# Optimization experiments

Measured on AMD Instinct MI355X. Metric: run time of the kernel, lower is better.

The kernel has to match this reference:

```python
import jax, jax.numpy as jnp
import numpy as np


def _gru_layer(x, h0, W_ih, W_hh, b_ih, b_hh):
    """PyTorch-convention GRU layer.
    x: [B, T, F], h0: [B, H], W_ih: [3H, F], W_hh: [3H, H], biases: [3H].
    Gate order (torch): r, z, n.  Returns (out [B,T,H], hT [B,H]).
    """
    # Precompute input projections for all timesteps in one big GEMM.
    gx = jnp.einsum('btf,gf->btg', x, W_ih) + b_ih  # [B, T, 3H]
    gx = jnp.swapaxes(gx, 0, 1)  # [T, B, 3H] for scan

    def step(h, gx_t):
        gh = h @ W_hh.T + b_hh                      # [B, 3H]
        xr, xz, xn = jnp.split(gx_t, 3, axis=-1)
        hr, hz, hn = jnp.split(gh, 3, axis=-1)
        r = jax.nn.sigmoid(xr + hr)
        z = jax.nn.sigmoid(xz + hz)
        n = jnp.tanh(xn + r * hn)
        h_new = (1.0 - z) * n + z * h
        return h_new, h_new

    hT, outs = jax.lax.scan(step, h0, gx)
    return jnp.swapaxes(outs, 0, 1), hT  # [B, T, H], [B, H]


def setup_inputs() -> dict:
    key = jax.random.key(0)
    ks = jax.random.split(key, 12)
    B, T, F, H, O = 256, 2000, 80, 64, 29
    s = 1.0 / np.sqrt(H)  # torch GRU/Linear init scale ~ U(-1/sqrt(H), 1/sqrt(H))
    u = lambda k, shp: jax.random.uniform(k, shp, jnp.float32, -s, s)
    return {
        'x': jax.random.normal(ks[0], (B, T, F), jnp.float32),
        'h': jnp.zeros((2, B, H), jnp.float32),
        'W_ih0': u(ks[1], (3 * H, F)),
        'W_hh0': u(ks[2], (3 * H, H)),
        'b_ih0': u(ks[3], (3 * H,)),
        'b_hh0': u(ks[4], (3 * H,)),
        'W_ih1': u(ks[5], (3 * H, H)),
        'W_hh1': u(ks[6], (3 * H, H)),
        'b_ih1': u(ks[7], (3 * H,)),
        'b_hh1': u(ks[8], (3 * H,)),
        'W_fc': u(ks[9], (O, H)),
        'b_fc': u(ks[10], (O,)),
    }


def reference(x, h, W_ih0, W_hh0, b_ih0, b_hh0, W_ih1, W_hh1, b_ih1, b_hh1, W_fc, b_fc):
    # Layer 0
    out0, h0T = _gru_layer(x, h[0], W_ih0, W_hh0, b_ih0, b_hh0)
    # Layer 1 (inter-layer dropout disabled: inference / eval mode)
    out1, h1T = _gru_layer(out0, h[1], W_ih1, W_hh1, b_ih1, b_hh1)
    hidden_state = jnp.stack([h0T, h1T], axis=0)  # [num_layers, B, H]
    # fc(relu(output[:, -1]))
    logits = jax.nn.relu(out1[:, -1]) @ W_fc.T + b_fc  # [B, O]
    return logits, hidden_state
```

## Files before the change

### kernel.cpp

```cpp
#include <hip/hip_runtime.h>

#define T_STEPS 2000
#define BATCH   256
#define F_IN    80
#define HDIM    64

template<int N> struct IC { static constexpr int v = N; };

typedef _Float16 h2 __attribute__((ext_vector_type(2)));
typedef _Float16 h8 __attribute__((ext_vector_type(8)));

union U8 { h8 v; h2 p[4]; };

__device__ __forceinline__ float sigm_f(float v) {
    float e = __expf(-v);
    return __builtin_amdgcn_rcpf(1.f + e);
}
__device__ __forceinline__ float tanh_f(float v) {
    v = fminf(fmaxf(v, -15.f), 15.f);
    float e = __expf(-2.f * v);
    return (1.f - e) * __builtin_amdgcn_rcpf(1.f + e);
}
__device__ __forceinline__ void barrier_lds() {
    __builtin_amdgcn_s_waitcnt(0xC07F);
    __builtin_amdgcn_s_barrier();
}
__device__ __forceinline__ float fdot2(h2 a, h2 b, float c) {
    return __builtin_amdgcn_fdot2(a, b, c, false);
}
__device__ __forceinline__ h2 mk2(float a, float b) {
    h2 r; r.x = (_Float16)a; r.y = (_Float16)b; return r;
}

__global__ __launch_bounds__(64, 2)
void gx_gemm(const float* __restrict__ x,
             const float* __restrict__ Wih0,
             const float* __restrict__ bih0,
             const float* __restrict__ bhh0,
             _Float16* __restrict__ gxp)
{
    const int j = threadIdx.x;
    const long total = (long)BATCH * T_STEPS;
    const long per   = total / gridDim.x;
    const long r0    = (long)blockIdx.x * per;
    const long r1    = r0 + per;

    h2 wr[40], wz[40], wn[40];
    {
        const float4* a4 = (const float4*)(Wih0 + (size_t)j * F_IN);
        const float4* b4 = (const float4*)(Wih0 + (size_t)(64 + j) * F_IN);
        const float4* c4 = (const float4*)(Wih0 + (size_t)(128 + j) * F_IN);
        #pragma unroll
        for (int k = 0; k < 20; ++k) {
            float4 va = a4[k], vb = b4[k], vc = c4[k];
            wr[2*k] = mk2(va.x, va.y); wr[2*k+1] = mk2(va.z, va.w);
            wz[2*k] = mk2(vb.x, vb.y); wz[2*k+1] = mk2(vb.z, vb.w);
            wn[2*k] = mk2(vc.x, vc.y); wn[2*k+1] = mk2(vc.z, vc.w);
        }
    }
    const float br = bih0[j]       + bhh0[j];
    const float bz = bih0[64 + j]  + bhh0[64 + j];
    const float bn = bih0[128 + j];

    __shared__ __align__(16) _Float16 xs[2][80];

    if (j < 40) {
        float2 v = ((const float2*)(x + r0 * F_IN))[j];
        *(h2*)&xs[0][2 * j] = mk2(v.x, v.y);
    }
    float2 vn = make_float2(0.f, 0.f);
    if (j < 40 && r0 + 1 < r1) vn = ((const float2*)(x + (r0 + 1) * F_IN))[j];

    for (long r = r0; r < r1; ++r) {
        const int cur = (int)(r - r0) & 1;
        float2 v2 = make_float2(0.f, 0.f);
        if (j < 40 && r + 2 < r1) v2 = ((const float2*)(x + (r + 2) * F_IN))[j];

        U8 xv[10];
        #pragma unroll
        for (int q = 0; q < 10; ++q) xv[q].v = ((const h8*)xs[cur])[q];

        float ar = br, az = bz, an = bn;
        #pragma unroll
        for (int q = 0; q < 10; ++q)
            #pragma unroll
            for (int p = 0; p < 4; ++p) {
                ar = fdot2(wr[4*q+p], xv[q].p[p], ar);
                az = fdot2(wz[4*q+p], xv[q].p[p], az);
                an = fdot2(wn[4*q+p], xv[q].p[p], an);
            }
        _Float16* g = gxp + r * 192;
        g[j]       = (_Float16)ar;
        g[64 + j]  = (_Float16)az;
        g[128 + j] = (_Float16)an;

        if (j < 40 && r + 1 < r1) *(h2*)&xs[cur ^ 1][2 * j] = mk2(vn.x, vn.y);
        vn = v2;
    }
}

__global__ __launch_bounds__(192, 1)
void gru_scan(const _Float16* __restrict__ gx,
              const float* __restrict__ hin,
              const float* __restrict__ Whh0,
              const float* __restrict__ bhh0,
              const float* __restrict__ Wih1,
              const float* __restrict__ Whh1,
              const float* __restrict__ bih1, const float* __restrict__ bhh1,
              float* __restrict__ out_hidden)
{
    const int b = blockIdx.x;
    const int j = threadIdx.x & 63;
    const int w = threadIdx.x >> 6;

    __shared__ __align__(16) _Float16 h0r[4][64];
    __shared__ __align__(16) _Float16 h1r[2][64];
    __shared__ __align__(16) float    pxs[2][3][64];

    if (w == 0) {
        h2 whr[32], whz[32], whn[32];
        {
            const float4* a4 = (const float4*)(Whh0 + (size_t)j * HDIM);
            const float4* b4 = (const float4*)(Whh0 + (size_t)(64 + j) * HDIM);
            const float4* c4 = (const float4*)(Whh0 + (size_t)(128 + j) * HDIM);
            #pragma unroll
            for (int k = 0; k < 16; ++k) {
                float4 va = a4[k], vb = b4[k], vc = c4[k];
                whr[2*k]=mk2(va.x,va.y); whr[2*k+1]=mk2(va.z,va.w);
                whz[2*k]=mk2(vb.x,vb.y); whz[2*k+1]=mk2(vb.z,vb.w);
                whn[2*k]=mk2(vc.x,vc.y); whn[2*k+1]=mk2(vc.z,vc.w);
            }
        }
        const float bn0h = bhh0[128 + j];
        float hreg = hin[b * HDIM + j];
        h0r[3][j] = (_Float16)hreg;
        U8 hv[8];
        #pragma unroll
        for (int q = 0; q < 8; ++q) hv[q].v = ((const h8*)h0r[3])[q];

        const _Float16* gbase = gx + (size_t)b * T_STEPS * 192;
        _Float16 grf[2], gzf[2], gnf[2];
        grf[0] = gbase[j];       gzf[0] = gbase[64 + j];       gnf[0] = gbase[128 + j];
        grf[1] = gbase[192 + j]; gzf[1] = gbase[192 + 64 + j]; gnf[1] = gbase[192 + 128 + j];

        __syncthreads();

        auto stepL0 = [&](int i, auto c3) {
            constexpr int I3 = decltype(c3)::v;
            constexpr int IP = I3 & 1;
            float ar  = (float)grf[IP];
            float az  = (float)gzf[IP];
            float gxn = (float)gnf[IP];
            float anh = bn0h;
            const int ipf = (i + 2 < T_STEPS) ? (i + 2) : (T_STEPS - 1);
            const _Float16* gnx = gbase + (size_t)ipf * 192 + j;
            grf[IP] = gnx[0]; gzf[IP] = gnx[64]; gnf[IP] = gnx[128];
            #pragma unroll
            for (int q = 0; q < 8; ++q)
                #pragma unroll
                for (int p = 0; p < 4; ++p) {
                    ar  = fdot2(whr[4*q+p], hv[q].p[p], ar);
                    az  = fdot2(whz[4*q+p], hv[q].p[p], az);
                    anh = fdot2(whn[4*q+p], hv[q].p[p], anh);
                }
            float r = sigm_f(ar);
            float z = sigm_f(az);
            float n = tanh_f(gxn + r * anh);
            hreg = (1.f - z) * n + z * hreg;
            h0r[I3][j] = (_Float16)hreg;
            #pragma unroll
            for (int q = 0; q < 8; ++q) hv[q].v = ((const h8*)h0r[I3])[q];
            barrier_lds();
        };

        stepL0(0, IC<0>{}); stepL0(1, IC<1>{}); stepL0(2, IC<2>{}); stepL0(3, IC<3>{});
        for (int ii = 1; ii < T_STEPS / 4; ++ii) {
            const int i = 4 * ii;
            stepL0(i + 0, IC<0>{}); stepL0(i + 1, IC<1>{});
            stepL0(i + 2, IC<2>{}); stepL0(i + 3, IC<3>{});
        }
        barrier_lds();
        out_hidden[b * HDIM + j] = hreg;
    } else if (w == 1) {
        h2 xr1[32], xz1[32], xn1[32];
        {
            const float4* a4 = (const float4*)(Wih1 + (size_t)j * HDIM);
            const float4* b4 = (const float4*)(Wih1 + (size_t)(64 + j) * HDIM);
            const float4* c4 = (const float4*)(Wih1 + (size_t)(128 + j) * HDIM);
            #pragma unroll
            for (int k = 0; k < 16; ++k) {
                float4 va = a4[k], vb = b4[k], vc = c4[k];
                xr1[2*k]=mk2(va.x,va.y); xr1[2*k+1]=mk2(va.z,va.w);
                xz1[2*k]=mk2(vb.x,vb.y); xz1[2*k+1]=mk2(vb.z,vb.w);
                xn1[2*k]=mk2(vc.x,vc.y); xn1[2*k+1]=mk2(vc.z,vc.w);
            }
        }
        const float brm = bih1[j] + bhh1[j];
        const float bzm = bih1[64 + j] + bhh1[64 + j];
        const float bnx = bih1[128 + j];

        __syncthreads();

        auto stepW1 = [&](auto c3) {
            constexpr int I3 = decltype(c3)::v;
            constexpr int IR = (I3 + 3) & 3;
            constexpr int PS = (I3 + 1) & 1;
            U8 hv[8];
            #pragma unroll
            for (int q = 0; q < 8; ++q) hv[q].v = ((const h8*)h0r[IR])[q];
            float ar = brm, az = bzm, an = bnx;
            #pragma unroll
            for (int q = 0; q < 8; ++q)
                #pragma unroll
                for (int p = 0; p < 4; ++p) {
                    ar = fdot2(xr1[4*q+p], hv[q].p[p], ar);
                    az = fdot2(xz1[4*q+p], hv[q].p[p], az);
                    an = fdot2(xn1[4*q+p], hv[q].p[p], an);
                }
            pxs[PS][0][j] = ar;
            pxs[PS][1][j] = az;
            pxs[PS][2][j] = an;
            barrier_lds();
        };

        barrier_lds();
        stepW1(IC<1>{}); stepW1(IC<2>{}); stepW1(IC<3>{});
        for (int ii = 1; ii < T_STEPS / 4; ++ii) {
            stepW1(IC<0>{}); stepW1(IC<1>{});
            stepW1(IC<2>{}); stepW1(IC<3>{});
        }
        stepW1(IC<0>{});
    } else {
        h2 hr1[32], hz1[32], hn1[32];
        {
            const float4* a4 = (const float4*)(Whh1 + (size_t)j * HDIM);
            const float4* b4 = (const float4*)(Whh1 + (size_t)(64 + j) * HDIM);
            const float4* c4 = (const float4*)(Whh1 + (size_t)(128 + j) * HDIM);
            #pragma unroll
            for (int k = 0; k < 16; ++k) {
                float4 va = a4[k], vb = b4[k], vc = c4[k];
                hr1[2*k]=mk2(va.x,va.y); hr1[2*k+1]=mk2(va.z,va.w);
                hz1[2*k]=mk2(vb.x,vb.y); hz1[2*k+1]=mk2(vb.z,vb.w);
                hn1[2*k]=mk2(vc.x,vc.y); hn1[2*k+1]=mk2(vc.z,vc.w);
            }
        }
        const float bnh = bhh1[128 + j];
        float hreg = hin[BATCH * HDIM + b * HDIM + j];
        h1r[1][j] = (_Float16)hreg;
        U8 uv[8];
        #pragma unroll
        for (int q = 0; q < 8; ++q) uv[q].v = ((const h8*)h1r[1])[q];

        __syncthreads();

        auto stepW2 = [&](auto c3) {
            constexpr int I3 = decltype(c3)::v;
            constexpr int IP = I3 & 1;
            const float pr = pxs[IP][0][j];
            const float pz = pxs[IP][1][j];
            const float pn = pxs[IP][2][j];
            float ahr = 0.f, ahz = 0.f, anh = bnh;
            #pragma unroll
            for (int q = 0; q < 8; ++q)
                #pragma unroll
                for (int p = 0; p < 4; ++p) {
                    ahr = fdot2(hr1[4*q+p], uv[q].p[p], ahr);
                    ahz = fdot2(hz1[4*q+p], uv[q].p[p], ahz);
                    anh = fdot2(hn1[4*q+p], uv[q].p[p], anh);
                }
            float r = sigm_f(pr + ahr);
            float z = sigm_f(pz + ahz);
            float n = tanh_f(pn + r * anh);
            hreg = (1.f - z) * n + z * hreg;
            h1r[IP][j] = (_Float16)hreg;
            #pragma unroll
            for (int q = 0; q < 8; ++q) uv[q].v = ((const h8*)h1r[IP])[q];
            barrier_lds();
        };

        barrier_lds(); barrier_lds();
        stepW2(IC<2>{}); stepW2(IC<3>{});
        for (int ii = 1; ii < T_STEPS / 4; ++ii) {
            stepW2(IC<0>{}); stepW2(IC<1>{});
            stepW2(IC<2>{}); stepW2(IC<3>{});
        }
        stepW2(IC<0>{});
        {
            const float pr = pxs[1][0][j];
            const float pz = pxs[1][1][j];
            const float pn = pxs[1][2][j];
            float ahr = 0.f, ahz = 0.f, anh = bnh;
            #pragma unroll
            for (int q = 0; q < 8; ++q)
                #pragma unroll
                for (int p = 0; p < 4; ++p) {
                    ahr = fdot2(hr1[4*q+p], uv[q].p[p], ahr);
                    ahz = fdot2(hz1[4*q+p], uv[q].p[p], ahz);
                    anh = fdot2(hn1[4*q+p], uv[q].p[p], anh);
                }
            float r = sigm_f(pr + ahr);
            float z = sigm_f(pz + ahz);
            float n = tanh_f(pn + r * anh);
            hreg = (1.f - z) * n + z * hreg;
        }
        out_hidden[BATCH * HDIM + b * HDIM + j] = hreg;
    }
}

__global__ void fc_kernel(const float* __restrict__ hidden,
                          const float* __restrict__ Wfc,
                          const float* __restrict__ bfc,
                          float* __restrict__ logits)
{
    const int b = blockIdx.x;
    const int o = threadIdx.x;
    if (o < 29) {
        const float* hb = hidden + BATCH * HDIM + b * HDIM;
        float acc = bfc[o];
        #pragma unroll
        for (int j = 0; j < HDIM; ++j)
            acc += fmaxf(hb[j], 0.f) * Wfc[o * HDIM + j];
        logits[b * 29 + o] = acc;
    }
}

extern "C" void kernel_launch(void* const* d_in, const int* in_sizes, int n_in,
                              void* d_out, int out_size, void* d_ws, size_t ws_size,
                              hipStream_t stream) {
    const float* x    = (const float*)d_in[0];
    const float* h    = (const float*)d_in[1];
    const float* Wih0 = (const float*)d_in[2];
    const float* Whh0 = (const float*)d_in[3];
    const float* bih0 = (const float*)d_in[4];
    const float* bhh0 = (const float*)d_in[5];
    const float* Wih1 = (const float*)d_in[6];
    const float* Whh1 = (const float*)d_in[7];
    const float* bih1 = (const float*)d_in[8];
    const float* bhh1 = (const float*)d_in[9];
    const float* Wfc  = (const float*)d_in[10];
    const float* bfc  = (const float*)d_in[11];

    float* out    = (float*)d_out;
    float* logits = out;
    float* hidden = out + BATCH * 29;

    _Float16* gxp = (_Float16*)d_ws;

    gx_gemm<<<2048, 64, 0, stream>>>(x, Wih0, bih0, bhh0, gxp);
    gru_scan<<<BATCH, 192, 0, stream>>>(
        gxp, h, Whh0, bhh0, Wih1, Whh1, bih1, bhh1, hidden);
    fc_kernel<<<BATCH, 64, 0, stream>>>(hidden, Wfc, bfc, logits);
}
```

Baseline: 1.122 ms.

## Batch two GRU timesteps per barrier in the wavefront-specialized scan pipeline

The three-wavefront scan (layer-0 recurrence, layer-1 input projection, layer-1 recurrence) now advances two timesteps between block barriers instead of one. The layer-0 and layer-1 waves run two dependent steps back to back inside one wave, and the projection wave fills a four-slot pxs buffer two steps at a time. This halves the barrier count along the serial critical path, at the cost of more pipeline stages and more LDS buffers. Separately, the gx GEMM launches twice as many blocks and moves its next-row LDS staging store ahead of the dot products.

Result: slower. 1.203 ms (+7.2%).

```diff
diff --git a/kernel.cpp b/kernel.cpp
--- a/kernel.cpp
+++ b/kernel.cpp
@@ -31,6 +31,28 @@
 __device__ __forceinline__ h2 mk2(float a, float b) {
     h2 r; r.x = (_Float16)a; r.y = (_Float16)b; return r;
 }
+
+#define DOT96(WR, WZ, WN, HA, HB, AR, AZ, AN)                 \
+    {                                                          \
+        _Pragma("unroll")                                      \
+        for (int q = 0; q < 4; ++q) {                          \
+            _Pragma("unroll")                                  \
+            for (int pp = 0; pp < 4; ++pp) {                   \
+                AR = fdot2(WR[4*q+pp], HA[q].p[pp], AR);       \
+                AZ = fdot2(WZ[4*q+pp], HA[q].p[pp], AZ);       \
+                AN = fdot2(WN[4*q+pp], HA[q].p[pp], AN);       \
+            }                                                  \
+        }                                                      \
+        _Pragma("unroll")                                      \
+        for (int q = 0; q < 4; ++q) {                          \
+            _Pragma("unroll")                                  \
+            for (int pp = 0; pp < 4; ++pp) {                   \
+                AR = fdot2(WR[16+4*q+pp], HB[q].p[pp], AR);    \
+                AZ = fdot2(WZ[16+4*q+pp], HB[q].p[pp], AZ);    \
+                AN = fdot2(WN[16+4*q+pp], HB[q].p[pp], AN);    \
+            }                                                  \
+        }                                                      \
+    }
 
 __global__ __launch_bounds__(64, 2)
 void gx_gemm(const float* __restrict__ x,
@@ -80,22 +102,22 @@
         #pragma unroll
         for (int q = 0; q < 10; ++q) xv[q].v = ((const h8*)xs[cur])[q];
 
+        if (j < 40 && r + 1 < r1) *(h2*)&xs[cur ^ 1][2 * j] = mk2(vn.x, vn.y);
+        vn = v2;
+
         float ar = br, az = bz, an = bn;
         #pragma unroll
         for (int q = 0; q < 10; ++q)
             #pragma unroll
-            for (int p = 0; p < 4; ++p) {
-                ar = fdot2(wr[4*q+p], xv[q].p[p], ar);
-                az = fdot2(wz[4*q+p], xv[q].p[p], az);
-                an = fdot2(wn[4*q+p], xv[q].p[p], an);
+            for (int pp = 0; pp < 4; ++pp) {
+                ar = fdot2(wr[4*q+pp], xv[q].p[pp], ar);
+                az = fdot2(wz[4*q+pp], xv[q].p[pp], az);
+                an = fdot2(wn[4*q+pp], xv[q].p[pp], an);
             }
         _Float16* g = gxp + r * 192;
         g[j]       = (_Float16)ar;
         g[64 + j]  = (_Float16)az;
         g[128 + j] = (_Float16)an;
-
-        if (j < 40 && r + 1 < r1) *(h2*)&xs[cur ^ 1][2 * j] = mk2(vn.x, vn.y);
-        vn = v2;
     }
 }
 
@@ -115,7 +137,7 @@
 
     __shared__ __align__(16) _Float16 h0r[4][64];
     __shared__ __align__(16) _Float16 h1r[2][64];
-    __shared__ __align__(16) float    pxs[2][3][64];
+    __shared__ __align__(16) float    pxs[4][3][64];
 
     if (w == 0) {
         h2 whr[32], whz[32], whn[32];
@@ -134,52 +156,72 @@
         const float bn0h = bhh0[128 + j];
         float hreg = hin[b * HDIM + j];
         h0r[3][j] = (_Float16)hreg;
-        U8 hv[8];
-        #pragma unroll
-        for (int q = 0; q < 8; ++q) hv[q].v = ((const h8*)h0r[3])[q];
 
         const _Float16* gbase = gx + (size_t)b * T_STEPS * 192;
-        _Float16 grf[2], gzf[2], gnf[2];
-        grf[0] = gbase[j];       gzf[0] = gbase[64 + j];       gnf[0] = gbase[128 + j];
-        grf[1] = gbase[192 + j]; gzf[1] = gbase[192 + 64 + j]; gnf[1] = gbase[192 + 128 + j];
+        _Float16 gxr[4], gxz[4], gxn[4];
+        #pragma unroll
+        for (int t = 0; t < 4; ++t) {
+            gxr[t] = gbase[t * 192 + j];
+            gxz[t] = gbase[t * 192 + 64 + j];
+            gxn[t] = gbase[t * 192 + 128 + j];
+        }
 
         __syncthreads();
 
-        auto stepL0 = [&](int i, auto c3) {
-            constexpr int I3 = decltype(c3)::v;
-            constexpr int IP = I3 & 1;
-            float ar  = (float)grf[IP];
-            float az  = (float)gzf[IP];
-            float gxn = (float)gnf[IP];
-            float anh = bn0h;
-            const int ipf = (i + 2 < T_STEPS) ? (i + 2) : (T_STEPS - 1);
-            const _Float16* gnx = gbase + (size_t)ipf * 192 + j;
-            grf[IP] = gnx[0]; gzf[IP] = gnx[64]; gnf[IP] = gnx[128];
-            #pragma unroll
-            for (int q = 0; q < 8; ++q)
-                #pragma unroll
-                for (int p = 0; p < 4; ++p) {
-                    ar  = fdot2(whr[4*q+p], hv[q].p[p], ar);
-                    az  = fdot2(whz[4*q+p], hv[q].p[p], az);
-                    anh = fdot2(whn[4*q+p], hv[q].p[p], anh);
+        U8 hA0[4], hB0[4];
+        #pragma unroll
+        for (int q = 0; q < 4; ++q) hA0[q].v = ((const h8*)h0r[3])[q];
+        #pragma unroll
+        for (int q = 0; q < 4; ++q) hB0[q].v = ((const h8*)h0r[3])[4 + q];
+
+        auto superW0 = [&](int S, auto cA) {
+            constexpr int A = decltype(cA)::v;
+            constexpr int B2 = A + 1;
+            if (S < 1000) {
+                const int t0 = 2 * S;
+                float gr = (float)gxr[A], gz = (float)gxz[A], gn = (float)gxn[A];
+                {
+                    const int tp = (t0 + 4 < T_STEPS) ? (t0 + 4) : (T_STEPS - 1);
+                    const _Float16* gp = gbase + (size_t)tp * 192 + j;
+                    gxr[A] = gp[0]; gxz[A] = gp[64]; gxn[A] = gp[128];
                 }
-            float r = sigm_f(ar);
-            float z = sigm_f(az);
-            float n = tanh_f(gxn + r * anh);
-            hreg = (1.f - z) * n + z * hreg;
-            h0r[I3][j] = (_Float16)hreg;
-            #pragma unroll
-            for (int q = 0; q < 8; ++q) hv[q].v = ((const h8*)h0r[I3])[q];
+                float ar = 0.f, az = 0.f, an = 0.f;
+                DOT96(whr, whz, whn, hA0, hB0, ar, az, an);
+                float r = sigm_f(gr + ar);
+                float z = sigm_f(gz + az);
+                float n = tanh_f(gn + r * (bn0h + an));
+                hreg = (1.f - z) * n + z * hreg;
+                h0r[A][j] = (_Float16)hreg;
+                U8 hA1[4], hB1[4];
+                #pragma unroll
+                for (int q = 0; q < 4; ++q) hA1[q].v = ((const h8*)h0r[A])[q];
+                #pragma unroll
+                for (int q = 0; q < 4; ++q) hB1[q].v = ((const h8*)h0r[A])[4 + q];
+                float gr1 = (float)gxr[B2], gz1 = (float)gxz[B2], gn1 = (float)gxn[B2];
+                {
+                    const int tp = (t0 + 5 < T_STEPS) ? (t0 + 5) : (T_STEPS - 1);
+                    const _Float16* gp = gbase + (size_t)tp * 192 + j;
+                    gxr[B2] = gp[0]; gxz[B2] = gp[64]; gxn[B2] = gp[128];
+                }
+                float ar1 = 0.f, az1 = 0.f, an1 = 0.f;
+                DOT96(whr, whz, whn, hA1, hB1, ar1, az1, an1);
+                float r1 = sigm_f(gr1 + ar1);
+                float z1 = sigm_f(gz1 + az1);
+                float n1 = tanh_f(gn1 + r1 * (bn0h + an1));
+                hreg = (1.f - z1) * n1 + z1 * hreg;
+                h0r[B2][j] = (_Float16)hreg;
+                #pragma unroll
+                for (int q = 0; q < 4; ++q) hA0[q].v = ((const h8*)h0r[B2])[q];
+                #pragma unroll
+                for (int q = 0; q < 4; ++q) hB0[q].v = ((const h8*)h0r[B2])[4 + q];
+            }
             barrier_lds();
         };
 
-        stepL0(0, IC<0>{}); stepL0(1, IC<1>{}); stepL0(2, IC<2>{}); stepL0(3, IC<3>{});
-        for (int ii = 1; ii < T_STEPS / 4; ++ii) {
-            const int i = 4 * ii;
-            stepL0(i + 0, IC<0>{}); stepL0(i + 1, IC<1>{});
-            stepL0(i + 2, IC<2>{}); stepL0(i + 3, IC<3>{});
-        }
-        barrier_lds();
+        for (int si = 0; si <= 500; ++si) {
+            superW0(2 * si,     IC<0>{});
+            superW0(2 * si + 1, IC<2>{});
+        }
         out_hidden[b * HDIM + j] = hreg;
     } else if (w == 1) {
         h2 xr1[32], xz1[32], xn1[32];
@@ -201,35 +243,37 @@
 
         __syncthreads();
 
-        auto stepW1 = [&](auto c3) {
-            constexpr int I3 = decltype(c3)::v;
-            constexpr int IR = (I3 + 3) & 3;
-            constexpr int PS = (I3 + 1) & 1;
-            U8 hv[8];
-            #pragma unroll
-            for (int q = 0; q < 8; ++q) hv[q].v = ((const h8*)h0r[IR])[q];
-            float ar = brm, az = bzm, an = bnx;
-            #pragma unroll
-            for (int q = 0; q < 8; ++q)
-                #pragma unroll
-                for (int p = 0; p < 4; ++p) {
-                    ar = fdot2(xr1[4*q+p], hv[q].p[p], ar);
-                    az = fdot2(xz1[4*q+p], hv[q].p[p], az);
-                    an = fdot2(xn1[4*q+p], hv[q].p[p], an);
-                }
-            pxs[PS][0][j] = ar;
-            pxs[PS][1][j] = az;
-            pxs[PS][2][j] = an;
+        auto superW1 = [&](int S, auto cH) {
+            constexpr int H0 = decltype(cH)::v;
+            constexpr int H1 = H0 + 1;
+            if (S >= 1 && S <= 1000) {
+                U8 a0[4], b0[4], a1[4], b1[4];
+                #pragma unroll
+                for (int q = 0; q < 4; ++q) a0[q].v = ((const h8*)h0r[H0])[q];
+                #pragma unroll
+                for (int q = 0; q < 4; ++q) b0[q].v = ((const h8*)h0r[H0])[4 + q];
+                #pragma unroll
+                for (int q = 0; q < 4; ++q) a1[q].v = ((const h8*)h0r[H1])[q];
+                #pragma unroll
+                for (int q = 0; q < 4; ++q) b1[q].v = ((const h8*)h0r[H1])[4 + q];
+                float ar = 0.f, az = 0.f, an = 0.f;
+                DOT96(xr1, xz1, xn1, a0, b0, ar, az, an);
+                pxs[H0][0][j] = brm + ar;
+                pxs[H0][1][j] = bzm + az;
+                pxs[H0][2][j] = bnx + an;
+                float ar1 = 0.f, az1 = 0.f, an1 = 0.f;
+                DOT96(xr1, xz1, xn1, a1, b1, ar1, az1, an1);
+                pxs[H1][0][j] = brm + ar1;
+                pxs[H1][1][j] = bzm + az1;
+                pxs[H1][2][j] = bnx + an1;
+            }
             barrier_lds();
         };
 
-        barrier_lds();
-        stepW1(IC<1>{}); stepW1(IC<2>{}); stepW1(IC<3>{});
-        for (int ii = 1; ii < T_STEPS / 4; ++ii) {
-            stepW1(IC<0>{}); stepW1(IC<1>{});
-            stepW1(IC<2>{}); stepW1(IC<3>{});
-        }
-        stepW1(IC<0>{});
+        for (int si = 0; si <= 500; ++si) {
+            superW1(2 * si,     IC<2>{});
+            superW1(2 * si + 1, IC<0>{});
+        }
     } else {
         h2 hr1[32], hz1[32], hn1[32];
         {
@@ -247,61 +291,55 @@
         const float bnh = bhh1[128 + j];
         float hreg = hin[BATCH * HDIM + b * HDIM + j];
         h1r[1][j] = (_Float16)hreg;
-        U8 uv[8];
-        #pragma unroll
-        for (int q = 0; q < 8; ++q) uv[q].v = ((const h8*)h1r[1])[q];
 
         __syncthreads();
 
-        auto stepW2 = [&](auto c3) {
-            constexpr int I3 = decltype(c3)::v;
-            constexpr int IP = I3 & 1;
-            const float pr = pxs[IP][0][j];
-            const float pz = pxs[IP][1][j];
-            const float pn = pxs[IP][2][j];
-            float ahr = 0.f, ahz = 0.f, anh = bnh;
-            #pragma unroll
-            for (int q = 0; q < 8; ++q)
-                #pragma unroll
-                for (int p = 0; p < 4; ++p) {
-                    ahr = fdot2(hr1[4*q+p], uv[q].p[p], ahr);
-                    ahz = fdot2(hz1[4*q+p], uv[q].p[p], ahz);
-                    anh = fdot2(hn1[4*q+p], uv[q].p[p], anh);
-                }
-            float r = sigm_f(pr + ahr);
-            float z = sigm_f(pz + ahz);
-            float n = tanh_f(pn + r * anh);
-            hreg = (1.f - z) * n + z * hreg;
-            h1r[IP][j] = (_Float16)hreg;
-            #pragma unroll
-            for (int q = 0; q < 8; ++q) uv[q].v = ((const h8*)h1r[IP])[q];
+        U8 uA[4], uB[4];
+        #pragma unroll
+        for (int q = 0; q < 4; ++q) uA[q].v = ((const h8*)h1r[1])[q];
+        #pragma unroll
+        for (int q = 0; q < 4; ++q) uB[q].v = ((const h8*)h1r[1])[4 + q];
+
+        auto superW2 = [&](int S, auto cP) {
+            constexpr int P0 = decltype(cP)::v;
+            constexpr int P1 = P0 + 1;
+            if (S >= 2) {
+                const float pr0 = pxs[P0][0][j];
+                const float pz0 = pxs[P0][1][j];
+                const float pn0 = pxs[P0][2][j];
+                const float pr1 = pxs[P1][0][j];
+                const float pz1 = pxs[P1][1][j];
+                const float pn1 = pxs[P1][2][j];
+                float ar = 0.f, az = 0.f, an = 0.f;
+                DOT96(hr1, hz1, hn1, uA, uB, ar, az, an);
+                float r = sigm_f(pr0 + ar);
+                float z = sigm_f(pz0 + az);
+                float n = tanh_f(pn0 + r * (bnh + an));
+                hreg = (1.f - z) * n + z * hreg;
+                h1r[0][j] = (_Float16)hreg;
+                U8 vA[4], vB[4];
+                #pragma unroll
+                for (int q = 0; q < 4; ++q) vA[q].v = ((const h8*)h1r[0])[q];
+                #pragma unroll
+                for (int q = 0; q < 4; ++q) vB[q].v = ((const h8*)h1r[0])[4 + q];
+                float ar1 = 0.f, az1 = 0.f, an1 = 0.f;
+                DOT96(hr1, hz1, hn1, vA, vB, ar1, az1, an1);
+                float r1 = sigm_f(pr1 + ar1);
+                float z1 = sigm_f(pz1 + az1);
+                float n1 = tanh_f(pn1 + r1 * (bnh + an1));
+                hreg = (1.f - z1) * n1 + z1 * hreg;
+                h1r[1][j] = (_Float16)hreg;
+                #pragma unroll
+                for (int q = 0; q < 4; ++q) uA[q].v = ((const h8*)h1r[1])[q];
+                #pragma unroll
+                for (int q = 0; q < 4; ++q) uB[q].v = ((const h8*)h1r[1])[4 + q];
+            }
             barrier_lds();
         };
 
-        barrier_lds(); barrier_lds();
-        stepW2(IC<2>{}); stepW2(IC<3>{});
-        for (int ii = 1; ii < T_STEPS / 4; ++ii) {
-            stepW2(IC<0>{}); stepW2(IC<1>{});
-            stepW2(IC<2>{}); stepW2(IC<3>{});
-        }
-        stepW2(IC<0>{});
-        {
-            const float pr = pxs[1][0][j];
-            const float pz = pxs[1][1][j];
-            const float pn = pxs[1][2][j];
-            float ahr = 0.f, ahz = 0.f, anh = bnh;
-            #pragma unroll
-            for (int q = 0; q < 8; ++q)
-                #pragma unroll
-                for (int p = 0; p < 4; ++p) {
-                    ahr = fdot2(hr1[4*q+p], uv[q].p[p], ahr);
-                    ahz = fdot2(hz1[4*q+p], uv[q].p[p], ahz);
-                    anh = fdot2(hn1[4*q+p], uv[q].p[p], anh);
-                }
-            float r = sigm_f(pr + ahr);
-            float z = sigm_f(pz + ahz);
-            float n = tanh_f(pn + r * anh);
-            hreg = (1.f - z) * n + z * hreg;
+        for (int si = 0; si <= 500; ++si) {
+            superW2(2 * si,     IC<0>{});
+            superW2(2 * si + 1, IC<2>{});
         }
         out_hidden[BATCH * HDIM + b * HDIM + j] = hreg;
     }
@@ -346,7 +384,7 @@
 
     _Float16* gxp = (_Float16*)d_ws;
 
-    gx_gemm<<<2048, 64, 0, stream>>>(x, Wih0, bih0, bhh0, gxp);
+    gx_gemm<<<4096, 64, 0, stream>>>(x, Wih0, bih0, bhh0, gxp);
     gru_scan<<<BATCH, 192, 0, stream>>>(
         gxp, h, Whh0, bhh0, Wih1, Whh1, bih1, bhh1, hidden);
     fc_kernel<<<BATCH, 64, 0, stream>>>(hidden, Wfc, bfc, logits);
```

## Split recurrent dot-product chains and process two rows per iteration in gx GEMM

Applied to the files above, without the earlier changes.

In the scan kernel, each gate's 32-deep dependent fdot2 chain is split into two independent 16-deep accumulators, which shortens the serial latency on the recurrent critical path. The hidden-state LDS reload moves from after the write to the start of the next step. The input-projection GEMM now computes two rows per iteration with a four-slot LDS ring and deeper prefetch, and the grid doubles from 2048 to 4096 blocks. The extra accumulators and doubled row buffers raise register pressure, and the reduction order for the gates changes.

Result: no change. 1.107 ms (-1.3%).

```diff
diff --git a/kernel.cpp b/kernel.cpp
--- a/kernel.cpp
+++ b/kernel.cpp
@@ -31,6 +31,22 @@
 __device__ __forceinline__ h2 mk2(float a, float b) {
     h2 r; r.x = (_Float16)a; r.y = (_Float16)b; return r;
 }
+
+#define DOT96_6(WR, WZ, WN, HA, HB, ARA, ARB, AZA, AZB, ANA, ANB)   \
+    {                                                                \
+        _Pragma("unroll")                                            \
+        for (int q = 0; q < 4; ++q) {                                \
+            _Pragma("unroll")                                        \
+            for (int pp = 0; pp < 4; ++pp) {                         \
+                ARA = fdot2(WR[4*q+pp],    HA[q].p[pp], ARA);        \
+                ARB = fdot2(WR[16+4*q+pp], HB[q].p[pp], ARB);        \
+                AZA = fdot2(WZ[4*q+pp],    HA[q].p[pp], AZA);        \
+                AZB = fdot2(WZ[16+4*q+pp], HB[q].p[pp], AZB);        \
+                ANA = fdot2(WN[4*q+pp],    HA[q].p[pp], ANA);        \
+                ANB = fdot2(WN[16+4*q+pp], HB[q].p[pp], ANB);        \
+            }                                                        \
+        }                                                            \
+    }
 
 __global__ __launch_bounds__(64, 2)
 void gx_gemm(const float* __restrict__ x,
@@ -62,40 +78,76 @@
     const float bz = bih0[64 + j]  + bhh0[64 + j];
     const float bn = bih0[128 + j];
 
-    __shared__ __align__(16) _Float16 xs[2][80];
-
-    if (j < 40) {
-        float2 v = ((const float2*)(x + r0 * F_IN))[j];
-        *(h2*)&xs[0][2 * j] = mk2(v.x, v.y);
-    }
-    float2 vn = make_float2(0.f, 0.f);
-    if (j < 40 && r0 + 1 < r1) vn = ((const float2*)(x + (r0 + 1) * F_IN))[j];
-
-    for (long r = r0; r < r1; ++r) {
-        const int cur = (int)(r - r0) & 1;
-        float2 v2 = make_float2(0.f, 0.f);
-        if (j < 40 && r + 2 < r1) v2 = ((const float2*)(x + (r + 2) * F_IN))[j];
-
-        U8 xv[10];
-        #pragma unroll
-        for (int q = 0; q < 10; ++q) xv[q].v = ((const h8*)xs[cur])[q];
-
-        float ar = br, az = bz, an = bn;
+    __shared__ __align__(16) _Float16 xs[4][80];
+
+    const bool ld = (j < 40);
+    if (ld) {
+        float2 v0 = ((const float2*)(x + r0 * F_IN))[j];
+        float2 v1 = ((const float2*)(x + (r0 + 1) * F_IN))[j];
+        *(h2*)&xs[0][2 * j] = mk2(v0.x, v0.y);
+        *(h2*)&xs[1][2 * j] = mk2(v1.x, v1.y);
+    }
+    float2 vA = make_float2(0.f, 0.f), vB = make_float2(0.f, 0.f);
+    if (ld && r0 + 2 < r1) vA = ((const float2*)(x + (r0 + 2) * F_IN))[j];
+    if (ld && r0 + 3 < r1) vB = ((const float2*)(x + (r0 + 3) * F_IN))[j];
+
+    long r = r0;
+    for (; r + 1 < r1; r += 2) {
+        float2 v4 = make_float2(0.f, 0.f), v5 = make_float2(0.f, 0.f);
+        if (ld && r + 4 < r1) v4 = ((const float2*)(x + (r + 4) * F_IN))[j];
+        if (ld && r + 5 < r1) v5 = ((const float2*)(x + (r + 5) * F_IN))[j];
+
+        const int s0 = (int)(r - r0) & 3, s1 = (s0 + 1) & 3;
+        U8 x0[10], x1[10];
+        #pragma unroll
+        for (int q = 0; q < 10; ++q) {
+            x0[q].v = ((const h8*)xs[s0])[q];
+            x1[q].v = ((const h8*)xs[s1])[q];
+        }
+        if (ld && r + 2 < r1) *(h2*)&xs[(s0 + 2) & 3][2 * j] = mk2(vA.x, vA.y);
+        if (ld && r + 3 < r1) *(h2*)&xs[(s0 + 3) & 3][2 * j] = mk2(vB.x, vB.y);
+        vA = v4; vB = v5;
+
+        float ar0 = br, az0 = bz, an0 = bn;
+        float ar1 = br, az1 = bz, an1 = bn;
         #pragma unroll
         for (int q = 0; q < 10; ++q)
             #pragma unroll
-            for (int p = 0; p < 4; ++p) {
-                ar = fdot2(wr[4*q+p], xv[q].p[p], ar);
-                az = fdot2(wz[4*q+p], xv[q].p[p], az);
-                an = fdot2(wn[4*q+p], xv[q].p[p], an);
-            }
-        _Float16* g = gxp + r * 192;
-        g[j]       = (_Float16)ar;
-        g[64 + j]  = (_Float16)az;
-        g[128 + j] = (_Float16)an;
-
-        if (j < 40 && r + 1 < r1) *(h2*)&xs[cur ^ 1][2 * j] = mk2(vn.x, vn.y);
-        vn = v2;
+            for (int pp = 0; pp < 4; ++pp) {
+                ar0 = fdot2(wr[4*q+pp], x0[q].p[pp], ar0);
+                ar1 = fdot2(wr[4*q+pp], x1[q].p[pp], ar1);
+                az0 = fdot2(wz[4*q+pp], x0[q].p[pp], az0);
+                az1 = fdot2(wz[4*q+pp], x1[q].p[pp], az1);
+                an0 = fdot2(wn[4*q+pp], x0[q].p[pp], an0);
+                an1 = fdot2(wn[4*q+pp], x1[q].p[pp], an1);
+            }
+        _Float16* g0 = gxp + r * 192;
+        _Float16* g1 = gxp + (r + 1) * 192;
+        g0[j]       = (_Float16)ar0;
+        g0[64 + j]  = (_Float16)az0;
+        g0[128 + j] = (_Float16)an0;
+        g1[j]       = (_Float16)ar1;
+        g1[64 + j]  = (_Float16)az1;
+        g1[128 + j] = (_Float16)an1;
+    }
+    if (r < r1) {
+        const int s0 = (int)(r - r0) & 3;
+        U8 x0[10];
+        #pragma unroll
+        for (int q = 0; q < 10; ++q) x0[q].v = ((const h8*)xs[s0])[q];
+        float ar0 = br, az0 = bz, an0 = bn;
+        #pragma unroll
+        for (int q = 0; q < 10; ++q)
+            #pragma unroll
+            for (int pp = 0; pp < 4; ++pp) {
+                ar0 = fdot2(wr[4*q+pp], x0[q].p[pp], ar0);
+                az0 = fdot2(wz[4*q+pp], x0[q].p[pp], az0);
+                an0 = fdot2(wn[4*q+pp], x0[q].p[pp], an0);
+            }
+        _Float16* g0 = gxp + r * 192;
+        g0[j]       = (_Float16)ar0;
+        g0[64 + j]  = (_Float16)az0;
+        g0[128 + j] = (_Float16)an0;
     }
 }
 
@@ -134,9 +186,6 @@
         const float bn0h = bhh0[128 + j];
         float hreg = hin[b * HDIM + j];
         h0r[3][j] = (_Float16)hreg;
-        U8 hv[8];
-        #pragma unroll
-        for (int q = 0; q < 8; ++q) hv[q].v = ((const h8*)h0r[3])[q];
 
         const _Float16* gbase = gx + (size_t)b * T_STEPS * 192;
         _Float16 grf[2], gzf[2], gnf[2];
@@ -148,33 +197,31 @@
         auto stepL0 = [&](int i, auto c3) {
             constexpr int I3 = decltype(c3)::v;
             constexpr int IP = I3 & 1;
-            float ar  = (float)grf[IP];
-            float az  = (float)gzf[IP];
-            float gxn = (float)gnf[IP];
-            float anh = bn0h;
+            constexpr int IR = (I3 + 3) & 3;
+            U8 hA[4], hB[4];
+            #pragma unroll
+            for (int q = 0; q < 4; ++q) {
+                hA[q].v = ((const h8*)h0r[IR])[q];
+                hB[q].v = ((const h8*)h0r[IR])[4 + q];
+            }
+            float gr = (float)grf[IP];
+            float gz = (float)gzf[IP];
+            float gn = (float)gnf[IP];
             const int ipf = (i + 2 < T_STEPS) ? (i + 2) : (T_STEPS - 1);
             const _Float16* gnx = gbase + (size_t)ipf * 192 + j;
             grf[IP] = gnx[0]; gzf[IP] = gnx[64]; gnf[IP] = gnx[128];
-            #pragma unroll
-            for (int q = 0; q < 8; ++q)
-                #pragma unroll
-                for (int p = 0; p < 4; ++p) {
-                    ar  = fdot2(whr[4*q+p], hv[q].p[p], ar);
-                    az  = fdot2(whz[4*q+p], hv[q].p[p], az);
-                    anh = fdot2(whn[4*q+p], hv[q].p[p], anh);
-                }
-            float r = sigm_f(ar);
-            float z = sigm_f(az);
-            float n = tanh_f(gxn + r * anh);
+
+            float arA = 0.f, arB = 0.f, azA = 0.f, azB = 0.f, anA = 0.f, anB = 0.f;
+            DOT96_6(whr, whz, whn, hA, hB, arA, arB, azA, azB, anA, anB);
+            float r = sigm_f(gr + (arA + arB));
+            float z = sigm_f(gz + (azA + azB));
+            float n = tanh_f(gn + r * (bn0h + (anA + anB)));
             hreg = (1.f - z) * n + z * hreg;
             h0r[I3][j] = (_Float16)hreg;
-            #pragma unroll
-            for (int q = 0; q < 8; ++q) hv[q].v = ((const h8*)h0r[I3])[q];
             barrier_lds();
         };
 
-        stepL0(0, IC<0>{}); stepL0(1, IC<1>{}); stepL0(2, IC<2>{}); stepL0(3, IC<3>{});
-        for (int ii = 1; ii < T_STEPS / 4; ++ii) {
+        for (int ii = 0; ii < T_STEPS / 4; ++ii) {
             const int i = 4 * ii;
             stepL0(i + 0, IC<0>{}); stepL0(i + 1, IC<1>{});
             stepL0(i + 2, IC<2>{}); stepL0(i + 3, IC<3>{});
@@ -205,21 +252,17 @@
             constexpr int I3 = decltype(c3)::v;
             constexpr int IR = (I3 + 3) & 3;
             constexpr int PS = (I3 + 1) & 1;
-            U8 hv[8];
-            #pragma unroll
-            for (int q = 0; q < 8; ++q) hv[q].v = ((const h8*)h0r[IR])[q];
-            float ar = brm, az = bzm, an = bnx;
-            #pragma unroll
-            for (int q = 0; q < 8; ++q)
-                #pragma unroll
-                for (int p = 0; p < 4; ++p) {
-                    ar = fdot2(xr1[4*q+p], hv[q].p[p], ar);
-                    az = fdot2(xz1[4*q+p], hv[q].p[p], az);
-                    an = fdot2(xn1[4*q+p], hv[q].p[p], an);
-                }
-            pxs[PS][0][j] = ar;
-            pxs[PS][1][j] = az;
-            pxs[PS][2][j] = an;
+            U8 hA[4], hB[4];
+            #pragma unroll
+            for (int q = 0; q < 4; ++q) {
+                hA[q].v = ((const h8*)h0r[IR])[q];
+                hB[q].v = ((const h8*)h0r[IR])[4 + q];
+            }
+            float arA = 0.f, arB = 0.f, azA = 0.f, azB = 0.f, anA = 0.f, anB = 0.f;
+            DOT96_6(xr1, xz1, xn1, hA, hB, arA, arB, azA, azB, anA, anB);
+            pxs[PS][0][j] = brm + (arA + arB);
+            pxs[PS][1][j] = bzm + (azA + azB);
+            pxs[PS][2][j] = bnx + (anA + anB);
             barrier_lds();
         };
 
@@ -247,34 +290,29 @@
         const float bnh = bhh1[128 + j];
         float hreg = hin[BATCH * HDIM + b * HDIM + j];
         h1r[1][j] = (_Float16)hreg;
-        U8 uv[8];
-        #pragma unroll
-        for (int q = 0; q < 8; ++q) uv[q].v = ((const h8*)h1r[1])[q];
 
         __syncthreads();
 
         auto stepW2 = [&](auto c3) {
             constexpr int I3 = decltype(c3)::v;
             constexpr int IP = I3 & 1;
+            constexpr int IU = IP ^ 1;
             const float pr = pxs[IP][0][j];
             const float pz = pxs[IP][1][j];
             const float pn = pxs[IP][2][j];
-            float ahr = 0.f, ahz = 0.f, anh = bnh;
-            #pragma unroll
-            for (int q = 0; q < 8; ++q)
-                #pragma unroll
-                for (int p = 0; p < 4; ++p) {
-                    ahr = fdot2(hr1[4*q+p], uv[q].p[p], ahr);
-                    ahz = fdot2(hz1[4*q+p], uv[q].p[p], ahz);
-                    anh = fdot2(hn1[4*q+p], uv[q].p[p], anh);
-                }
-            float r = sigm_f(pr + ahr);
-            float z = sigm_f(pz + ahz);
-            float n = tanh_f(pn + r * anh);
+            U8 hA[4], hB[4];
+            #pragma unroll
+            for (int q = 0; q < 4; ++q) {
+                hA[q].v = ((const h8*)h1r[IU])[q];
+                hB[q].v = ((const h8*)h1r[IU])[4 + q];
+            }
+            float arA = 0.f, arB = 0.f, azA = 0.f, azB = 0.f, anA = 0.f, anB = 0.f;
+            DOT96_6(hr1, hz1, hn1, hA, hB, arA, arB, azA, azB, anA, anB);
+            float r = sigm_f(pr + (arA + arB));
+            float z = sigm_f(pz + (azA + azB));
+            float n = tanh_f(pn + r * (bnh + (anA + anB)));
             hreg = (1.f - z) * n + z * hreg;
             h1r[IP][j] = (_Float16)hreg;
-            #pragma unroll
-            for (int q = 0; q < 8; ++q) uv[q].v = ((const h8*)h1r[IP])[q];
             barrier_lds();
         };
 
@@ -289,18 +327,17 @@
             const float pr = pxs[1][0][j];
             const float pz = pxs[1][1][j];
             const float pn = pxs[1][2][j];
-            float ahr = 0.f, ahz = 0.f, anh = bnh;
-            #pragma unroll
-            for (int q = 0; q < 8; ++q)
-                #pragma unroll
-                for (int p = 0; p < 4; ++p) {
-                    ahr = fdot2(hr1[4*q+p], uv[q].p[p], ahr);
-                    ahz = fdot2(hz1[4*q+p], uv[q].p[p], ahz);
-                    anh = fdot2(hn1[4*q+p], uv[q].p[p], anh);
-                }
-            float r = sigm_f(pr + ahr);
-            float z = sigm_f(pz + ahz);
-            float n = tanh_f(pn + r * anh);
+            U8 hA[4], hB[4];
+            #pragma unroll
+            for (int q = 0; q < 4; ++q) {
+                hA[q].v = ((const h8*)h1r[0])[q];
+                hB[q].v = ((const h8*)h1r[0])[4 + q];
+            }
+            float arA = 0.f, arB = 0.f, azA = 0.f, azB = 0.f, anA = 0.f, anB = 0.f;
+            DOT96_6(hr1, hz1, hn1, hA, hB, arA, arB, azA, azB, anA, anB);
+            float r = sigm_f(pr + (arA + arB));
+            float z = sigm_f(pz + (azA + azB));
+            float n = tanh_f(pn + r * (bnh + (anA + anB)));
             hreg = (1.f - z) * n + z * hreg;
         }
         out_hidden[BATCH * HDIM + b * HDIM + j] = hreg;
@@ -346,7 +383,7 @@
 
     _Float16* gxp = (_Float16*)d_ws;
 
-    gx_gemm<<<2048, 64, 0, stream>>>(x, Wih0, bih0, bhh0, gxp);
+    gx_gemm<<<4096, 64, 0, stream>>>(x, Wih0, bih0, bhh0, gxp);
     gru_scan<<<BATCH, 192, 0, stream>>>(
         gxp, h, Whh0, bhh0, Wih1, Whh1, bih1, bhh1, hidden);
     fc_kernel<<<BATCH, 64, 0, stream>>>(hidden, Wfc, bfc, logits);
```
